# Kernel optimization log

Measured on AMD Instinct MI355X. Metric: run time of the kernel, lower is better.

The kernel has to match this reference:

```python
import jax, jax.numpy as jnp
import numpy as np

B, A, C, M = 8, 32768, 80, 32
VAR0, VAR1 = 0.1, 0.2          # cfg['variance']
TOPK = 50                      # pre_anchor_topk
T1 = 0.5                       # bbox_threshold
SL1_W, SL1_B = 0.75, 0.11      # smooth_l1_loss_param
ALPHA, GAMMA = 0.5, 2.0
EPS = 1e-12


def point_form(b):
    # center form (cx,cy,w,h) -> corner form (x0,y0,x1,y1)
    return jnp.concatenate([b[..., :2] - b[..., 2:] / 2,
                            b[..., :2] + b[..., 2:] / 2], axis=-1)


def decode(loc, priors):
    xy = priors[..., :2] + loc[..., :2] * VAR0 * priors[..., 2:]
    wh = priors[..., 2:] * jnp.exp(loc[..., 2:] * VAR1)
    return jnp.concatenate([xy, wh], axis=-1)  # center form


def encode(matched, priors):
    # matched: corner form, priors: center form
    g_xy = ((matched[..., :2] + matched[..., 2:]) / 2 - priors[..., :2]) / (VAR0 * priors[..., 2:])
    g_wh = jnp.log((matched[..., 2:] - matched[..., :2]) / priors[..., 2:]) / VAR1
    return jnp.concatenate([g_xy, g_wh], axis=-1)


def jaccard(a, b):
    # a: [M,4] corner, b: [A,4] corner -> IoU [M,A]
    lt = jnp.maximum(a[:, None, :2], b[None, :, :2])
    rb = jnp.minimum(a[:, None, 2:], b[None, :, 2:])
    wh = jnp.clip(rb - lt, 0.0, None)
    inter = wh[..., 0] * wh[..., 1]
    area_a = (a[:, 2] - a[:, 0]) * (a[:, 3] - a[:, 1])
    area_b = (b[:, 2] - b[:, 0]) * (b[:, 3] - b[:, 1])
    return inter / (area_a[:, None] + area_b[None, :] - inter)


def clip_st(x, lo):
    # Clip custom Function: straight-through gradient
    return x + jax.lax.stop_gradient(jnp.maximum(x, lo) - x)


def bce_log(x):
    # torch BCE clamps log at -100
    return jnp.maximum(jnp.log(jnp.clip(x, 1e-38, None)), -100.0)


def _per_image(box_reg, cls_p, tgt, lab, anchors, num_classes):
    # ---- image_box_prob (no-grad branch in original) ----
    decoded = point_form(decode(box_reg, anchors))          # [A,4]
    obi = jaccard(tgt, decoded)                             # [M,A]
    t2 = jnp.maximum(obi.max(axis=1, keepdims=True), T1 + EPS)
    obp = jnp.clip((obi - T1) / (t2 - T1), 0.0, 1.0)        # [M,A]
    # sparse per-class max over objects == segment_max on labels
    seg = jax.ops.segment_max(obp, lab, num_segments=num_classes)  # [C,A]
    image_box_prob = jax.lax.stop_gradient(jnp.maximum(seg, 0.0).T)  # [A,C]

    # ---- positive bag loss ----
    mq = jaccard(tgt, point_form(anchors))                  # [M,A]
    _, matched = jax.lax.top_k(mq, TOPK)                    # [M,K]
    cls_sel = cls_p[:, lab].T                               # [M,A] prob of own class
    matched_cls = jnp.take_along_axis(cls_sel, matched, axis=1)  # [M,K]
    pri = anchors[matched]                                  # [M,K,4]
    tgt_enc = encode(tgt[:, None, :], pri)                  # [M,K,4]
    val = tgt_enc - box_reg[matched]
    av = jnp.abs(val)
    reg_loss = SL1_W * jnp.where(av < SL1_B, 0.5 / SL1_B * val * val, av - 0.5 * SL1_B).sum(-1)
    logits = matched_cls * jnp.exp(-reg_loss)               # [M,K]
    w = 1.0 / clip_st(1.0 - logits, EPS)
    w = w / w.sum(axis=1, keepdims=True)
    bag = (w * logits).sum(axis=1)                          # [M]
    pos = -bce_log(bag)                                     # BCE(bag, 1)
    return image_box_prob, pos


def setup_inputs() -> dict:
    key = jax.random.key(0)
    k1, k2, k3, k4, k5, k6, k7 = jax.random.split(key, 7)
    box_regression = jax.random.normal(k1, (B, A, 4), jnp.float32) * 0.5
    cls_logits = jax.random.normal(k2, (B, A, C), jnp.float32) - 2.0
    a_xy = jax.random.uniform(k3, (A, 2))
    a_wh = 0.02 + 0.2 * jax.random.uniform(k4, (A, 2))
    anchors = jnp.concatenate([a_xy, a_wh], axis=-1).astype(jnp.float32)
    t_min = 0.5 * jax.random.uniform(k5, (B, M, 2))
    t_wh = 0.05 + 0.4 * jax.random.uniform(k6, (B, M, 2))
    target_boxes = jnp.concatenate([t_min, t_min + t_wh], axis=-1).astype(jnp.float32)
    labels = jax.random.randint(k7, (B, M), 0, C, dtype=jnp.int32)
    return {"box_regression": box_regression, "cls_logits": cls_logits,
            "anchors": anchors, "target_boxes": target_boxes, "labels": labels}


def reference(box_regression, cls_logits, anchors, target_boxes, labels):
    num_classes = cls_logits.shape[-1]
    cls_prob = jax.nn.sigmoid(cls_logits)                   # [B,A,C]
    box_prob, pos = jax.vmap(
        lambda br, cp, tb, lb: _per_image(br, cp, tb, lb, anchors, num_classes)
    )(box_regression, cls_prob, target_boxes, labels)       # [B,A,C], [B,M]
    positive_numels = target_boxes.shape[0] * target_boxes.shape[1]
    positive_loss = pos.sum() / max(1, positive_numels)
    p = cls_prob * (1.0 - box_prob)
    # focal_loss(p, gamma) = sum(p**gamma * BCE(p, 0)) = sum(p**gamma * -log(1-p))
    negative_loss = jnp.sum(p ** GAMMA * (-bce_log(1.0 - p))) / max(1, positive_numels * TOPK)
    return (positive_loss * ALPHA, negative_loss * (1.0 - ALPHA))
```

## Files before the change

### kernel.cpp

```cpp
#include <hip/hip_runtime.h>

#define NB 8
#define NA 32768
#define NC 80
#define NM 32
#define NK 50
#define CAP 2048
#define TB 32
#define HALF_A (NA / 2)
#define NBLK 1024
#define CORRB (NA / 256)
constexpr float VAR0 = 0.1f, VAR1 = 0.2f;
constexpr float T1f  = 0.5f;
constexpr float SL1B = 0.11f;
constexpr float SL1W = 0.75f;
constexpr float FEPS = 1e-12f;

__device__ __forceinline__ float iou_corner(float tx0, float ty0, float tx1, float ty1, float ta,
                                            float bx0, float by0, float bx1, float by1, float ba) {
  float lx = fmaxf(tx0, bx0), ly = fmaxf(ty0, by0);
  float rx = fminf(tx1, bx1), ry = fminf(ty1, by1);
  float wx = fmaxf(rx - lx, 0.f), wy = fmaxf(ry - ly, 0.f);
  float inter = wx * wy;
  return inter / (ta + ba - inter);
}

__device__ __forceinline__ float focal_term(float s, float bp) {
  float pr = s * (1.f - bp);
  float om = fmaxf(1.f - pr, 1e-38f);
  return pr * pr * fminf(-__logf(om), 100.f);
}

__device__ __forceinline__ float focal4(float4 v) {
  float s0 = 1.f / (1.f + __expf(-v.x));
  float s1 = 1.f / (1.f + __expf(-v.y));
  float s2 = 1.f / (1.f + __expf(-v.z));
  float s3 = 1.f / (1.f + __expf(-v.w));
  return focal_term(s0, 0.f) + focal_term(s1, 0.f) + focal_term(s2, 0.f) + focal_term(s3, 0.f);
}

__global__ void __launch_bounds__(1024, 8) mega_kernel(const float4* __restrict__ br,
                                                       const float* __restrict__ cls,
                                                       const float4* __restrict__ anc,
                                                       const float4* __restrict__ tgt,
                                                       unsigned* __restrict__ partmax,
                                                       unsigned* __restrict__ pairmask,
                                                       unsigned long long* __restrict__ cand50,
                                                       unsigned* __restrict__ poscnt,
                                                       unsigned* __restrict__ zlist,
                                                       unsigned* __restrict__ zcnt,
                                                       float* __restrict__ f0part) {
  __shared__ int hist[512];
  __shared__ unsigned long long cand[CAP];
  __shared__ int s_cnt, s_B1, s_filled, s_zc;
  __shared__ unsigned char s_flag[1024];
  __shared__ unsigned s_max[NM];
  __shared__ float4 s_t[NM];
  __shared__ float s_ta[NM];
  __shared__ float swave[16];

  int bx = blockIdx.x;
  int tid = threadIdx.x;

  {
    const float4* cls4 = (const float4*)cls;
    constexpr int STRIDE = NBLK * 1024;
    int base = bx * 1024 + tid;
    float4 v0 = cls4[base + 0 * STRIDE];
    float4 v1 = cls4[base + 1 * STRIDE];
    float4 v2 = cls4[base + 2 * STRIDE];
    float4 v3 = cls4[base + 3 * STRIDE];
    float4 v4 = cls4[base + 4 * STRIDE];
    float accum = focal4(v0) + focal4(v1) + focal4(v2) + focal4(v3) + focal4(v4);
    for (int off = 32; off; off >>= 1) accum += __shfl_down(accum, off);
    if ((tid & 63) == 0) swave[tid >> 6] = accum;
    __syncthreads();
    if (tid == 0) {
      float s = 0.f;
#pragma unroll
      for (int i = 0; i < 16; ++i) s += swave[i];
      f0part[bx] = s;
    }
    __syncthreads();
  }

  if (bx < 2 * NB * NM) {
    int bm = bx >> 1;
    int half = bx & 1;
    int abase = half * HALF_A;
    float4 t = tgt[bm];
    float ta = (t.z - t.x) * (t.w - t.y);

    if (tid < 512) hist[tid] = 0;
    if (tid == 0) s_cnt = 0;
    __syncthreads();

    float riou[16];
    unsigned mask = 0u;
#pragma unroll
    for (int k = 0; k < 16; ++k) {
      float4 p = anc[abase + tid + (k << 10)];
      float hx = 0.5f * p.z, hy = 0.5f * p.w;
      float x0 = p.x - hx, y0 = p.y - hy, x1 = p.x + hx, y1 = p.y + hy;
      float ba = (x1 - x0) * (y1 - y0);
      float v = iou_corner(t.x, t.y, t.z, t.w, ta, x0, y0, x1, y1, ba);
      riou[k] = v;
      if (v > 0.f) {
        mask |= 1u << k;
        atomicAdd(&hist[(int)(__float_as_uint(v) >> 21)], 1);
      }
    }
    __syncthreads();

    if (tid == 0) {
      int cum = 0, b1 = 0;
      for (int bin = 511; bin >= 0; --bin) {
        cum += hist[bin];
        if (cum >= NK) { b1 = bin; break; }
      }
      s_B1 = b1;
      s_filled = cum;
    }
    __syncthreads();
    int B1 = s_B1;
    int local_pos = s_filled;
    if (tid == 0) poscnt[bm * 2 + half] = (unsigned)min(local_pos, NK);

#pragma unroll
    for (int k = 0; k < 16; ++k) {
      float v = riou[k];
      if (v > 0.f) {
        unsigned vb = __float_as_uint(v);
        if ((int)(vb >> 21) >= B1) {
          int slot = atomicAdd(&s_cnt, 1);
          if (slot < CAP)
            cand[slot] = ((unsigned long long)vb << 32) | (unsigned)(~(abase + tid + (k << 10)));
        }
      }
    }
    __syncthreads();
    int n = min(s_cnt, CAP);

    for (int c = tid; c < n; c += 1024) {
      unsigned long long key = cand[c];
      int rank = 0;
      for (int j = 0; j < n; ++j) rank += (cand[j] > key);
      if (rank < NK) cand50[(size_t)(bm * 2 + half) * NK + rank] = key;
    }
    int nw = min(n, NK);
    if (tid >= nw && tid < NK)
      cand50[(size_t)(bm * 2 + half) * NK + tid] = 0ull;

    if (local_pos < NK) {
      if (tid == 0) s_zc = 0;
      __syncthreads();
#pragma unroll
      for (int k = 0; k < 16; ++k) {
        s_flag[tid] = ((mask >> k) & 1u) == 0u;
        __syncthreads();
        if (tid == 0) {
          for (int i = 0; i < 1024 && s_zc < NK; ++i)
            if (s_flag[i]) zlist[(size_t)(bm * 2 + half) * NK + s_zc++] = abase + (k << 10) + i;
        }
        __syncthreads();
      }
      if (tid == 0) zcnt[bm * 2 + half] = (unsigned)s_zc;
    }

  } else if (bx < 2 * NB * NM + TB * NB) {
    int t2i = bx - 2 * NB * NM;
    int b = t2i >> 5;
    int chunk = t2i & 31;
    if (tid < NM) {
      float4 t = tgt[b * NM + tid];
      s_t[tid] = t;
      s_ta[tid] = (t.z - t.x) * (t.w - t.y);
      s_max[tid] = 0u;
    }
    __syncthreads();

    int a = chunk * 1024 + tid;
    float4 p = anc[a];
    float4 l = br[(size_t)b * NA + a];
    float cx = p.x + l.x * VAR0 * p.z;
    float cy = p.y + l.y * VAR0 * p.w;
    float w = p.z * __expf(l.z * VAR1);
    float h = p.w * __expf(l.w * VAR1);
    float dx0 = cx - 0.5f * w, dy0 = cy - 0.5f * h;
    float dx1 = cx + 0.5f * w, dy1 = cy + 0.5f * h;
    float da = (dx1 - dx0) * (dy1 - dy0);

    unsigned mymask = 0u;
#pragma unroll
    for (int mm = 0; mm < NM; ++mm) {
      int m = (tid + mm) & (NM - 1);
      float4 t = s_t[m];
      float iou = iou_corner(t.x, t.y, t.z, t.w, s_ta[m], dx0, dy0, dx1, dy1, da);
      if (iou > T1f) mymask |= 1u << m;
      atomicMax(&s_max[m], __float_as_uint(iou));
    }
    pairmask[(size_t)b * NA + a] = mymask;
    __syncthreads();
    if (tid < NM)
      partmax[((size_t)b * NM + tid) * TB + chunk] = s_max[tid];
  }
}

__global__ void __launch_bounds__(128) posfin_kernel(const float4* __restrict__ br,
                                                     const float* __restrict__ cls,
                                                     const float4* __restrict__ anc,
                                                     const float4* __restrict__ tgt,
                                                     const int* __restrict__ labels,
                                                     const unsigned long long* __restrict__ cand50,
                                                     const unsigned* __restrict__ poscnt,
                                                     const unsigned* __restrict__ zlist,
                                                     const unsigned* __restrict__ zcnt,
                                                     float* __restrict__ posp) {
  __shared__ unsigned long long kbuf[2 * NK];
  __shared__ int sel[NK];
  __shared__ int s_total;
  int bm = blockIdx.x;
  int b = bm >> 5;
  int tid = threadIdx.x;
  float4 t = tgt[bm];

  if (tid < NK) {
    kbuf[tid]      = cand50[(size_t)(bm * 2 + 0) * NK + tid];
    kbuf[NK + tid] = cand50[(size_t)(bm * 2 + 1) * NK + tid];
  }
  if (tid == 0)
    s_total = (int)(poscnt[bm * 2] + poscnt[bm * 2 + 1]);
  __syncthreads();

  if (tid < 2 * NK) {
    unsigned long long key = kbuf[tid];
    if (key != 0ull) {
      int rank = 0;
      for (int j = 0; j < 2 * NK; ++j) rank += (kbuf[j] > key);
      if (rank < NK) sel[rank] = (int)(~(unsigned)(key & 0xFFFFFFFFull));
    }
  }
  __syncthreads();

  int total = s_total;
  if (total < NK) {
    if (tid == 0) {
      int idx = total;
      unsigned zc0 = zcnt[bm * 2], zc1 = zcnt[bm * 2 + 1];
      for (unsigned j = 0; j < zc0 && idx < NK; ++j) sel[idx++] = (int)zlist[(size_t)(bm * 2) * NK + j];
      for (unsigned j = 0; j < zc1 && idx < NK; ++j) sel[idx++] = (int)zlist[(size_t)(bm * 2 + 1) * NK + j];
    }
    __syncthreads();
  }

  if (tid < 64) {
    int lane = tid;
    float lg = 0.f, wr = 0.f;
    if (lane < NK) {
      int a = sel[lane];
      int lb = labels[bm];
      float4 p = anc[a];
      float4 l = br[(size_t)b * NA + a];
      float logit = cls[((size_t)b * NA + a) * NC + lb];
      float mc = 1.f / (1.f + __expf(-logit));
      float gx = ((t.x + t.z) * 0.5f - p.x) / (VAR0 * p.z);
      float gy = ((t.y + t.w) * 0.5f - p.y) / (VAR0 * p.w);
      float gw = __logf((t.z - t.x) / p.z) / VAR1;
      float gh = __logf((t.w - t.y) / p.w) / VAR1;
      float v0 = gx - l.x, v1 = gy - l.y, v2 = gw - l.z, v3 = gh - l.w;
      float rl = 0.f;
      {
        float av;
        av = fabsf(v0); rl += (av < SL1B) ? (0.5f / SL1B) * v0 * v0 : (av - 0.5f * SL1B);
        av = fabsf(v1); rl += (av < SL1B) ? (0.5f / SL1B) * v1 * v1 : (av - 0.5f * SL1B);
        av = fabsf(v2); rl += (av < SL1B) ? (0.5f / SL1B) * v2 * v2 : (av - 0.5f * SL1B);
        av = fabsf(v3); rl += (av < SL1B) ? (0.5f / SL1B) * v3 * v3 : (av - 0.5f * SL1B);
      }
      rl *= SL1W;
      lg = mc * __expf(-rl);
      wr = 1.f / fmaxf(1.f - lg, FEPS);
    }
    float swl = wr * lg, swr = wr;
    for (int off = 32; off; off >>= 1) { swl += __shfl_down(swl, off); swr += __shfl_down(swr, off); }
    if (lane == 0) {
      float bag = swl / swr;
      posp[bm] = -fmaxf(logf(fmaxf(bag, 1e-38f)), -100.f);
    }
  }
}

__global__ void __launch_bounds__(256) corr_kernel(const float4* __restrict__ br,
                                                   const float* __restrict__ cls,
                                                   const float4* __restrict__ anc,
                                                   const float4* __restrict__ tgt,
                                                   const int* __restrict__ labels,
                                                   const unsigned* __restrict__ partmax,
                                                   const unsigned* __restrict__ pairmask,
                                                   float* __restrict__ corrp) {
  __shared__ float4 s_t[NM];
  __shared__ float s_ta[NM], s_inv[NM];
  __shared__ unsigned s_cmask[NC];
  __shared__ unsigned s_maxm[NM];
  __shared__ unsigned s_slotmask[NM];
  __shared__ int s_slotclass[NM];
  __shared__ int s_nslots;
  int b = blockIdx.y;
  int tid = threadIdx.x;
  if (tid < NC) s_cmask[tid] = 0u;
  if (tid < NM) s_maxm[tid] = 0u;
  if (tid == 0) s_nslots = 0;
  __syncthreads();
  if (tid < NM) {
    float4 t = tgt[b * NM + tid];
    s_t[tid] = t;
    s_ta[tid] = (t.z - t.x) * (t.w - t.y);
    atomicOr(&s_cmask[labels[b * NM + tid]], 1u << tid);
  }
  {
    int m = tid >> 3, j = tid & 7;
    const unsigned* pm = &partmax[((size_t)b * NM + m) * TB];
    unsigned mx = 0u;
    for (int k = j; k < TB; k += 8) mx = max(mx, pm[k]);
    atomicMax(&s_maxm[m], mx);
  }
  __syncthreads();
  if (tid < NM) {
    float mxf = __uint_as_float(s_maxm[tid]);
    s_inv[tid] = 1.0f / (fmaxf(mxf, T1f) - T1f);
  }
  __syncthreads();
  if (tid < NC && s_cmask[tid] != 0u) {
    int slot = atomicAdd(&s_nslots, 1);
    s_slotmask[slot] = s_cmask[tid];
    s_slotclass[slot] = tid;
  }
  __syncthreads();
  int nslots = s_nslots;

  int a = blockIdx.x * 256 + tid;
  unsigned mk32 = pairmask[(size_t)b * NA + a];
  float accum = 0.f;
  if (mk32) {
    float4 p = anc[a];
    float4 l = br[(size_t)b * NA + a];
    float cx = p.x + l.x * VAR0 * p.z;
    float cy = p.y + l.y * VAR0 * p.w;
    float w = p.z * __expf(l.z * VAR1);
    float h = p.w * __expf(l.w * VAR1);
    float dx0 = cx - 0.5f * w, dy0 = cy - 0.5f * h;
    float dx1 = cx + 0.5f * w, dy1 = cy + 0.5f * h;
    float da = (dx1 - dx0) * (dy1 - dy0);
    for (int j = 0; j < nslots; ++j) {
      unsigned sm = mk32 & s_slotmask[j];
      if (!sm) continue;
      float bp = 0.f;
      while (sm) {
        int m = __ffs(sm) - 1;
        sm &= sm - 1;
        float4 t = s_t[m];
        float iou = iou_corner(t.x, t.y, t.z, t.w, s_ta[m], dx0, dy0, dx1, dy1, da);
        float o = (iou - T1f) * s_inv[m];
        bp = fmaxf(bp, fminf(fmaxf(o, 0.f), 1.f));
      }
      if (bp > 0.f) {
        float logit = cls[((size_t)b * NA + a) * NC + s_slotclass[j]];
        float s = 1.f / (1.f + __expf(-logit));
        accum += focal_term(s, bp) - focal_term(s, 0.f);
      }
    }
  }
  for (int off = 32; off; off >>= 1) accum += __shfl_down(accum, off);
  __shared__ float swv[4];
  if ((tid & 63) == 0) swv[tid >> 6] = accum;
  __syncthreads();
  if (tid == 0)
    corrp[(size_t)b * CORRB + blockIdx.x] = swv[0] + swv[1] + swv[2] + swv[3];
}

__global__ void __launch_bounds__(256) fin_kernel(const float* __restrict__ posp,
                                                  const float* __restrict__ f0part,
                                                  const float* __restrict__ corrp,
                                                  float* __restrict__ out) {
  int tid = threadIdx.x;
  double sp = 0.0, sn = 0.0;
  for (int i = tid; i < NB * NM; i += 256) sp += (double)posp[i];
  for (int i = tid; i < NBLK; i += 256) sn += (double)f0part[i];
  for (int i = tid; i < NB * CORRB; i += 256) sn += (double)corrp[i];
  for (int off = 32; off; off >>= 1) { sp += __shfl_down(sp, off); sn += __shfl_down(sn, off); }
  __shared__ double swp[4], swn[4];
  if ((tid & 63) == 0) { swp[tid >> 6] = sp; swn[tid >> 6] = sn; }
  __syncthreads();
  if (tid == 0) {
    double pos = swp[0] + swp[1] + swp[2] + swp[3];
    double neg = swn[0] + swn[1] + swn[2] + swn[3];
    out[0] = (float)(pos / 256.0 * 0.5);
    out[1] = (float)(neg / 12800.0 * 0.5);
  }
}

extern "C" void kernel_launch(void* const* d_in, const int* in_sizes, int n_in,
                              void* d_out, int out_size, void* d_ws, size_t ws_size,
                              hipStream_t stream) {
  const float4* br  = (const float4*)d_in[0];
  const float*  cls = (const float*)d_in[1];
  const float4* anc = (const float4*)d_in[2];
  const float4* tgt = (const float4*)d_in[3];
  const int*    lab = (const int*)d_in[4];
  float* out = (float*)d_out;
  float*              posp     = (float*)d_ws;
  float*              f0part   = (float*)((char*)d_ws + 4096);
  float*              corrp    = (float*)((char*)d_ws + 8192);
  unsigned*           poscnt   = (unsigned*)((char*)d_ws + 12288);
  unsigned*           partmax  = (unsigned*)((char*)d_ws + 16384);
  unsigned long long* cand50   = (unsigned long long*)((char*)d_ws + 49152);
  unsigned*           zlist    = (unsigned*)((char*)d_ws + 253952);
  unsigned*           zcnt     = (unsigned*)((char*)d_ws + 356352);
  unsigned*           pairmask = (unsigned*)((char*)d_ws + 360448);

  mega_kernel<<<dim3(NBLK), 1024, 0, stream>>>(
      br, cls, anc, tgt, partmax, pairmask, cand50, poscnt, zlist, zcnt, f0part);
  posfin_kernel<<<dim3(NB * NM), 128, 0, stream>>>(
      br, cls, anc, tgt, lab, cand50, poscnt, zlist, zcnt, posp);
  corr_kernel<<<dim3(CORRB, NB), 256, 0, stream>>>(br, cls, anc, tgt, lab, partmax, pairmask, corrp);
  fin_kernel<<<1, 256, 0, stream>>>(posp, f0part, corrp, out);
}
```

Measured before the change: 57.52 us.

## Merge four kernels into two with uniform mega blocks and last-block finalize

The mega kernel now runs 512 uniform blocks, and every block performs all three jobs: the dense focal sum over ten float4 loads per thread, decoded-box IoU for half the threads, and one top-k anchor selection. This replaces the earlier heterogeneous block roles. The positive-loss, correction and final-reduction kernels are folded into one tail kernel that accumulates into double atomics and finishes with a ticket-based last-block reduction. Candidate insertion now uses a wave ballot with one shared atomic per wave. The intent is fewer launches and better load balance, at the cost of more work serialized per block and reliance on global atomics and threadfence ordering.

```diff
diff --git a/kernel.cpp b/kernel.cpp
--- a/kernel.cpp
+++ b/kernel.cpp
@@ -6,10 +6,11 @@
 #define NM 32
 #define NK 50
 #define CAP 2048
-#define TB 32
 #define HALF_A (NA / 2)
-#define NBLK 1024
-#define CORRB (NA / 256)
+#define MBLK 512
+#define TPC 64
+#define CORR_BLOCKS (NB * 128)
+#define TAIL_BLOCKS (CORR_BLOCKS + NB * NM)
 constexpr float VAR0 = 0.1f, VAR1 = 0.2f;
 constexpr float T1f  = 0.5f;
 constexpr float SL1B = 0.11f;
@@ -49,7 +50,9 @@
                                                        unsigned* __restrict__ poscnt,
                                                        unsigned* __restrict__ zlist,
                                                        unsigned* __restrict__ zcnt,
-                                                       float* __restrict__ f0part) {
+                                                       float* __restrict__ f0part,
+                                                       double* __restrict__ acc,
+                                                       unsigned* __restrict__ ticket) {
   __shared__ int hist[512];
   __shared__ unsigned long long cand[CAP];
   __shared__ int s_cnt, s_B1, s_filled, s_zc;
@@ -62,9 +65,16 @@
   int bx = blockIdx.x;
   int tid = threadIdx.x;
 
+  if (bx == 0) {
+    if (tid < 16) acc[tid] = 0.0;
+    if (tid == 16) *ticket = 0u;
+  }
+
+  int b_img = bx >> 6;
+
   {
     const float4* cls4 = (const float4*)cls;
-    constexpr int STRIDE = NBLK * 1024;
+    constexpr int STRIDE = MBLK * 1024;
     int base = bx * 1024 + tid;
     float4 v0 = cls4[base + 0 * STRIDE];
     float4 v1 = cls4[base + 1 * STRIDE];
@@ -72,116 +82,34 @@
     float4 v3 = cls4[base + 3 * STRIDE];
     float4 v4 = cls4[base + 4 * STRIDE];
     float accum = focal4(v0) + focal4(v1) + focal4(v2) + focal4(v3) + focal4(v4);
+    float4 w0 = cls4[base + 5 * STRIDE];
+    float4 w1 = cls4[base + 6 * STRIDE];
+    float4 w2 = cls4[base + 7 * STRIDE];
+    float4 w3 = cls4[base + 8 * STRIDE];
+    float4 w4 = cls4[base + 9 * STRIDE];
+    accum += focal4(w0) + focal4(w1) + focal4(w2) + focal4(w3) + focal4(w4);
     for (int off = 32; off; off >>= 1) accum += __shfl_down(accum, off);
     if ((tid & 63) == 0) swave[tid >> 6] = accum;
-    __syncthreads();
-    if (tid == 0) {
-      float s = 0.f;
+  }
+  if (tid < NM) {
+    float4 t = tgt[b_img * NM + tid];
+    s_t[tid] = t;
+    s_ta[tid] = (t.z - t.x) * (t.w - t.y);
+    s_max[tid] = 0u;
+  }
+  __syncthreads();
+  if (tid == 0) {
+    float s = 0.f;
 #pragma unroll
-      for (int i = 0; i < 16; ++i) s += swave[i];
-      f0part[bx] = s;
-    }
-    __syncthreads();
-  }
-
-  if (bx < 2 * NB * NM) {
-    int bm = bx >> 1;
-    int half = bx & 1;
-    int abase = half * HALF_A;
-    float4 t = tgt[bm];
-    float ta = (t.z - t.x) * (t.w - t.y);
-
-    if (tid < 512) hist[tid] = 0;
-    if (tid == 0) s_cnt = 0;
-    __syncthreads();
-
-    float riou[16];
-    unsigned mask = 0u;
-#pragma unroll
-    for (int k = 0; k < 16; ++k) {
-      float4 p = anc[abase + tid + (k << 10)];
-      float hx = 0.5f * p.z, hy = 0.5f * p.w;
-      float x0 = p.x - hx, y0 = p.y - hy, x1 = p.x + hx, y1 = p.y + hy;
-      float ba = (x1 - x0) * (y1 - y0);
-      float v = iou_corner(t.x, t.y, t.z, t.w, ta, x0, y0, x1, y1, ba);
-      riou[k] = v;
-      if (v > 0.f) {
-        mask |= 1u << k;
-        atomicAdd(&hist[(int)(__float_as_uint(v) >> 21)], 1);
-      }
-    }
-    __syncthreads();
-
-    if (tid == 0) {
-      int cum = 0, b1 = 0;
-      for (int bin = 511; bin >= 0; --bin) {
-        cum += hist[bin];
-        if (cum >= NK) { b1 = bin; break; }
-      }
-      s_B1 = b1;
-      s_filled = cum;
-    }
-    __syncthreads();
-    int B1 = s_B1;
-    int local_pos = s_filled;
-    if (tid == 0) poscnt[bm * 2 + half] = (unsigned)min(local_pos, NK);
-
-#pragma unroll
-    for (int k = 0; k < 16; ++k) {
-      float v = riou[k];
-      if (v > 0.f) {
-        unsigned vb = __float_as_uint(v);
-        if ((int)(vb >> 21) >= B1) {
-          int slot = atomicAdd(&s_cnt, 1);
-          if (slot < CAP)
-            cand[slot] = ((unsigned long long)vb << 32) | (unsigned)(~(abase + tid + (k << 10)));
-        }
-      }
-    }
-    __syncthreads();
-    int n = min(s_cnt, CAP);
-
-    for (int c = tid; c < n; c += 1024) {
-      unsigned long long key = cand[c];
-      int rank = 0;
-      for (int j = 0; j < n; ++j) rank += (cand[j] > key);
-      if (rank < NK) cand50[(size_t)(bm * 2 + half) * NK + rank] = key;
-    }
-    int nw = min(n, NK);
-    if (tid >= nw && tid < NK)
-      cand50[(size_t)(bm * 2 + half) * NK + tid] = 0ull;
-
-    if (local_pos < NK) {
-      if (tid == 0) s_zc = 0;
-      __syncthreads();
-#pragma unroll
-      for (int k = 0; k < 16; ++k) {
-        s_flag[tid] = ((mask >> k) & 1u) == 0u;
-        __syncthreads();
-        if (tid == 0) {
-          for (int i = 0; i < 1024 && s_zc < NK; ++i)
-            if (s_flag[i]) zlist[(size_t)(bm * 2 + half) * NK + s_zc++] = abase + (k << 10) + i;
-        }
-        __syncthreads();
-      }
-      if (tid == 0) zcnt[bm * 2 + half] = (unsigned)s_zc;
-    }
-
-  } else if (bx < 2 * NB * NM + TB * NB) {
-    int t2i = bx - 2 * NB * NM;
-    int b = t2i >> 5;
-    int chunk = t2i & 31;
-    if (tid < NM) {
-      float4 t = tgt[b * NM + tid];
-      s_t[tid] = t;
-      s_ta[tid] = (t.z - t.x) * (t.w - t.y);
-      s_max[tid] = 0u;
-    }
-    __syncthreads();
-
-    int a = chunk * 1024 + tid;
+    for (int i = 0; i < 16; ++i) s += swave[i];
+    f0part[bx] = s;
+  }
+
+  if (tid >= 512) {
+    int g = bx * 512 + (tid - 512);
+    int a = g & (NA - 1);
     float4 p = anc[a];
-    float4 l = br[(size_t)b * NA + a];
+    float4 l = br[g];
     float cx = p.x + l.x * VAR0 * p.z;
     float cy = p.y + l.y * VAR0 * p.w;
     float w = p.z * __expf(l.z * VAR1);
@@ -189,7 +117,6 @@
     float dx0 = cx - 0.5f * w, dy0 = cy - 0.5f * h;
     float dx1 = cx + 0.5f * w, dy1 = cy + 0.5f * h;
     float da = (dx1 - dx0) * (dy1 - dy0);
-
     unsigned mymask = 0u;
 #pragma unroll
     for (int mm = 0; mm < NM; ++mm) {
@@ -199,202 +126,297 @@
       if (iou > T1f) mymask |= 1u << m;
       atomicMax(&s_max[m], __float_as_uint(iou));
     }
-    pairmask[(size_t)b * NA + a] = mymask;
-    __syncthreads();
-    if (tid < NM)
-      partmax[((size_t)b * NM + tid) * TB + chunk] = s_max[tid];
-  }
-}
-
-__global__ void __launch_bounds__(128) posfin_kernel(const float4* __restrict__ br,
-                                                     const float* __restrict__ cls,
-                                                     const float4* __restrict__ anc,
-                                                     const float4* __restrict__ tgt,
-                                                     const int* __restrict__ labels,
-                                                     const unsigned long long* __restrict__ cand50,
-                                                     const unsigned* __restrict__ poscnt,
-                                                     const unsigned* __restrict__ zlist,
-                                                     const unsigned* __restrict__ zcnt,
-                                                     float* __restrict__ posp) {
-  __shared__ unsigned long long kbuf[2 * NK];
-  __shared__ int sel[NK];
-  __shared__ int s_total;
-  int bm = blockIdx.x;
-  int b = bm >> 5;
-  int tid = threadIdx.x;
+    pairmask[g] = mymask;
+  }
+  if (tid < 512) hist[tid] = 0;
+  if (tid == 0) s_cnt = 0;
+  __syncthreads();
+  if (tid < NM)
+    partmax[((size_t)b_img * NM + tid) * TPC + (bx & 63)] = s_max[tid];
+
+  int bm = bx >> 1;
+  int half = bx & 1;
+  int abase = half * HALF_A;
   float4 t = tgt[bm];
-
-  if (tid < NK) {
-    kbuf[tid]      = cand50[(size_t)(bm * 2 + 0) * NK + tid];
-    kbuf[NK + tid] = cand50[(size_t)(bm * 2 + 1) * NK + tid];
-  }
-  if (tid == 0)
-    s_total = (int)(poscnt[bm * 2] + poscnt[bm * 2 + 1]);
-  __syncthreads();
-
-  if (tid < 2 * NK) {
-    unsigned long long key = kbuf[tid];
-    if (key != 0ull) {
-      int rank = 0;
-      for (int j = 0; j < 2 * NK; ++j) rank += (kbuf[j] > key);
-      if (rank < NK) sel[rank] = (int)(~(unsigned)(key & 0xFFFFFFFFull));
-    }
-  }
-  __syncthreads();
-
-  int total = s_total;
-  if (total < NK) {
-    if (tid == 0) {
-      int idx = total;
-      unsigned zc0 = zcnt[bm * 2], zc1 = zcnt[bm * 2 + 1];
-      for (unsigned j = 0; j < zc0 && idx < NK; ++j) sel[idx++] = (int)zlist[(size_t)(bm * 2) * NK + j];
-      for (unsigned j = 0; j < zc1 && idx < NK; ++j) sel[idx++] = (int)zlist[(size_t)(bm * 2 + 1) * NK + j];
-    }
-    __syncthreads();
-  }
-
-  if (tid < 64) {
-    int lane = tid;
-    float lg = 0.f, wr = 0.f;
-    if (lane < NK) {
-      int a = sel[lane];
-      int lb = labels[bm];
-      float4 p = anc[a];
-      float4 l = br[(size_t)b * NA + a];
-      float logit = cls[((size_t)b * NA + a) * NC + lb];
-      float mc = 1.f / (1.f + __expf(-logit));
-      float gx = ((t.x + t.z) * 0.5f - p.x) / (VAR0 * p.z);
-      float gy = ((t.y + t.w) * 0.5f - p.y) / (VAR0 * p.w);
-      float gw = __logf((t.z - t.x) / p.z) / VAR1;
-      float gh = __logf((t.w - t.y) / p.w) / VAR1;
-      float v0 = gx - l.x, v1 = gy - l.y, v2 = gw - l.z, v3 = gh - l.w;
-      float rl = 0.f;
-      {
-        float av;
-        av = fabsf(v0); rl += (av < SL1B) ? (0.5f / SL1B) * v0 * v0 : (av - 0.5f * SL1B);
-        av = fabsf(v1); rl += (av < SL1B) ? (0.5f / SL1B) * v1 * v1 : (av - 0.5f * SL1B);
-        av = fabsf(v2); rl += (av < SL1B) ? (0.5f / SL1B) * v2 * v2 : (av - 0.5f * SL1B);
-        av = fabsf(v3); rl += (av < SL1B) ? (0.5f / SL1B) * v3 * v3 : (av - 0.5f * SL1B);
-      }
-      rl *= SL1W;
-      lg = mc * __expf(-rl);
-      wr = 1.f / fmaxf(1.f - lg, FEPS);
-    }
-    float swl = wr * lg, swr = wr;
-    for (int off = 32; off; off >>= 1) { swl += __shfl_down(swl, off); swr += __shfl_down(swr, off); }
-    if (lane == 0) {
-      float bag = swl / swr;
-      posp[bm] = -fmaxf(logf(fmaxf(bag, 1e-38f)), -100.f);
-    }
-  }
-}
-
-__global__ void __launch_bounds__(256) corr_kernel(const float4* __restrict__ br,
+  float ta = (t.z - t.x) * (t.w - t.y);
+
+  float riou[16];
+  unsigned mask = 0u;
+#pragma unroll
+  for (int k = 0; k < 16; ++k) {
+    float4 p = anc[abase + tid + (k << 10)];
+    float hx = 0.5f * p.z, hy = 0.5f * p.w;
+    float x0 = p.x - hx, y0 = p.y - hy, x1 = p.x + hx, y1 = p.y + hy;
+    float ba = (x1 - x0) * (y1 - y0);
+    float v = iou_corner(t.x, t.y, t.z, t.w, ta, x0, y0, x1, y1, ba);
+    riou[k] = v;
+    if (v > 0.f) {
+      mask |= 1u << k;
+      atomicAdd(&hist[(int)(__float_as_uint(v) >> 21)], 1);
+    }
+  }
+  __syncthreads();
+
+  if (tid == 0) {
+    int cum = 0, b1 = 0;
+    for (int bin = 511; bin >= 0; --bin) {
+      cum += hist[bin];
+      if (cum >= NK) { b1 = bin; break; }
+    }
+    s_B1 = b1;
+    s_filled = cum;
+  }
+  __syncthreads();
+  int B1 = s_B1;
+  int local_pos = s_filled;
+  if (tid == 0) poscnt[bm * 2 + half] = (unsigned)min(local_pos, NK);
+
+  int lane = tid & 63;
+#pragma unroll
+  for (int k = 0; k < 16; ++k) {
+    float v = riou[k];
+    bool want = (v > 0.f) && ((int)(__float_as_uint(v) >> 21) >= B1);
+    unsigned long long ball = __ballot(want);
+    if (ball) {
+      int lead = __ffsll((long long)ball) - 1;
+      int base = 0;
+      if (lane == lead) base = atomicAdd(&s_cnt, __popcll(ball));
+      base = __shfl(base, lead);
+      if (want) {
+        int slot = base + __popcll(ball & ((1ull << lane) - 1ull));
+        if (slot < CAP)
+          cand[slot] = ((unsigned long long)__float_as_uint(v) << 32)
+                       | (unsigned)(~(abase + tid + (k << 10)));
+      }
+    }
+  }
+  __syncthreads();
+  int n = min(s_cnt, CAP);
+
+  for (int c = tid; c < n; c += 1024) {
+    unsigned long long key = cand[c];
+    int rank = 0;
+    for (int j = 0; j < n; ++j) rank += (cand[j] > key);
+    if (rank < NK) cand50[(size_t)(bm * 2 + half) * NK + rank] = key;
+  }
+  int nw = min(n, NK);
+  if (tid >= nw && tid < NK)
+    cand50[(size_t)(bm * 2 + half) * NK + tid] = 0ull;
+
+  if (local_pos < NK) {
+    if (tid == 0) s_zc = 0;
+    __syncthreads();
+#pragma unroll
+    for (int k = 0; k < 16; ++k) {
+      s_flag[tid] = ((mask >> k) & 1u) == 0u;
+      __syncthreads();
+      if (tid == 0) {
+        for (int i = 0; i < 1024 && s_zc < NK; ++i)
+          if (s_flag[i]) zlist[(size_t)(bm * 2 + half) * NK + s_zc++] = abase + (k << 10) + i;
+      }
+      __syncthreads();
+    }
+    if (tid == 0) zcnt[bm * 2 + half] = (unsigned)s_zc;
+  }
+}
+
+__global__ void __launch_bounds__(256) tail_kernel(const float4* __restrict__ br,
                                                    const float* __restrict__ cls,
                                                    const float4* __restrict__ anc,
                                                    const float4* __restrict__ tgt,
                                                    const int* __restrict__ labels,
                                                    const unsigned* __restrict__ partmax,
                                                    const unsigned* __restrict__ pairmask,
-                                                   float* __restrict__ corrp) {
-  __shared__ float4 s_t[NM];
-  __shared__ float s_ta[NM], s_inv[NM];
-  __shared__ unsigned s_cmask[NC];
-  __shared__ unsigned s_maxm[NM];
-  __shared__ unsigned s_slotmask[NM];
-  __shared__ int s_slotclass[NM];
-  __shared__ int s_nslots;
-  int b = blockIdx.y;
+                                                   const unsigned long long* __restrict__ cand50,
+                                                   const unsigned* __restrict__ poscnt,
+                                                   const unsigned* __restrict__ zlist,
+                                                   const unsigned* __restrict__ zcnt,
+                                                   const float* __restrict__ f0part,
+                                                   double* __restrict__ acc,
+                                                   unsigned* __restrict__ ticket,
+                                                   float* __restrict__ out) {
+  __shared__ int s_last;
+  int bx = blockIdx.x;
   int tid = threadIdx.x;
-  if (tid < NC) s_cmask[tid] = 0u;
-  if (tid < NM) s_maxm[tid] = 0u;
-  if (tid == 0) s_nslots = 0;
-  __syncthreads();
-  if (tid < NM) {
-    float4 t = tgt[b * NM + tid];
-    s_t[tid] = t;
-    s_ta[tid] = (t.z - t.x) * (t.w - t.y);
-    atomicOr(&s_cmask[labels[b * NM + tid]], 1u << tid);
-  }
-  {
-    int m = tid >> 3, j = tid & 7;
-    const unsigned* pm = &partmax[((size_t)b * NM + m) * TB];
-    unsigned mx = 0u;
-    for (int k = j; k < TB; k += 8) mx = max(mx, pm[k]);
-    atomicMax(&s_maxm[m], mx);
-  }
-  __syncthreads();
-  if (tid < NM) {
-    float mxf = __uint_as_float(s_maxm[tid]);
-    s_inv[tid] = 1.0f / (fmaxf(mxf, T1f) - T1f);
-  }
-  __syncthreads();
-  if (tid < NC && s_cmask[tid] != 0u) {
-    int slot = atomicAdd(&s_nslots, 1);
-    s_slotmask[slot] = s_cmask[tid];
-    s_slotclass[slot] = tid;
-  }
-  __syncthreads();
-  int nslots = s_nslots;
-
-  int a = blockIdx.x * 256 + tid;
-  unsigned mk32 = pairmask[(size_t)b * NA + a];
-  float accum = 0.f;
-  if (mk32) {
-    float4 p = anc[a];
-    float4 l = br[(size_t)b * NA + a];
-    float cx = p.x + l.x * VAR0 * p.z;
-    float cy = p.y + l.y * VAR0 * p.w;
-    float w = p.z * __expf(l.z * VAR1);
-    float h = p.w * __expf(l.w * VAR1);
-    float dx0 = cx - 0.5f * w, dy0 = cy - 0.5f * h;
-    float dx1 = cx + 0.5f * w, dy1 = cy + 0.5f * h;
-    float da = (dx1 - dx0) * (dy1 - dy0);
-    for (int j = 0; j < nslots; ++j) {
-      unsigned sm = mk32 & s_slotmask[j];
-      if (!sm) continue;
-      float bp = 0.f;
-      while (sm) {
-        int m = __ffs(sm) - 1;
-        sm &= sm - 1;
-        float4 t = s_t[m];
-        float iou = iou_corner(t.x, t.y, t.z, t.w, s_ta[m], dx0, dy0, dx1, dy1, da);
-        float o = (iou - T1f) * s_inv[m];
-        bp = fmaxf(bp, fminf(fmaxf(o, 0.f), 1.f));
-      }
-      if (bp > 0.f) {
-        float logit = cls[((size_t)b * NA + a) * NC + s_slotclass[j]];
-        float s = 1.f / (1.f + __expf(-logit));
-        accum += focal_term(s, bp) - focal_term(s, 0.f);
-      }
-    }
-  }
-  for (int off = 32; off; off >>= 1) accum += __shfl_down(accum, off);
-  __shared__ float swv[4];
-  if ((tid & 63) == 0) swv[tid >> 6] = accum;
-  __syncthreads();
-  if (tid == 0)
-    corrp[(size_t)b * CORRB + blockIdx.x] = swv[0] + swv[1] + swv[2] + swv[3];
-}
-
-__global__ void __launch_bounds__(256) fin_kernel(const float* __restrict__ posp,
-                                                  const float* __restrict__ f0part,
-                                                  const float* __restrict__ corrp,
-                                                  float* __restrict__ out) {
-  int tid = threadIdx.x;
-  double sp = 0.0, sn = 0.0;
-  for (int i = tid; i < NB * NM; i += 256) sp += (double)posp[i];
-  for (int i = tid; i < NBLK; i += 256) sn += (double)f0part[i];
-  for (int i = tid; i < NB * CORRB; i += 256) sn += (double)corrp[i];
-  for (int off = 32; off; off >>= 1) { sp += __shfl_down(sp, off); sn += __shfl_down(sn, off); }
-  __shared__ double swp[4], swn[4];
-  if ((tid & 63) == 0) { swp[tid >> 6] = sp; swn[tid >> 6] = sn; }
-  __syncthreads();
+
+  if (bx < CORR_BLOCKS) {
+    __shared__ float4 s_t[NM];
+    __shared__ float s_ta[NM], s_inv[NM];
+    __shared__ unsigned s_cmask[NC];
+    __shared__ unsigned s_maxm[NM];
+    __shared__ unsigned s_slotmask[NM];
+    __shared__ int s_slotclass[NM];
+    __shared__ int s_nslots;
+    int b = bx >> 7;
+    if (tid < NC) s_cmask[tid] = 0u;
+    if (tid < NM) s_maxm[tid] = 0u;
+    if (tid == 0) s_nslots = 0;
+    __syncthreads();
+    if (tid < NM) {
+      float4 t = tgt[b * NM + tid];
+      s_t[tid] = t;
+      s_ta[tid] = (t.z - t.x) * (t.w - t.y);
+      atomicOr(&s_cmask[labels[b * NM + tid]], 1u << tid);
+    }
+    {
+      int m = tid >> 3, j = tid & 7;
+      const unsigned* pm = &partmax[((size_t)b * NM + m) * TPC];
+      unsigned mx = 0u;
+      for (int k = j; k < TPC; k += 8) mx = max(mx, pm[k]);
+      atomicMax(&s_maxm[m], mx);
+    }
+    __syncthreads();
+    if (tid < NM) {
+      float mxf = __uint_as_float(s_maxm[tid]);
+      s_inv[tid] = 1.0f / (fmaxf(mxf, T1f) - T1f);
+    }
+    __syncthreads();
+    if (tid < NC && s_cmask[tid] != 0u) {
+      int slot = atomicAdd(&s_nslots, 1);
+      s_slotmask[slot] = s_cmask[tid];
+      s_slotclass[slot] = tid;
+    }
+    __syncthreads();
+    int nslots = s_nslots;
+
+    int a = (bx & 127) * 256 + tid;
+    unsigned mk32 = pairmask[(size_t)b * NA + a];
+    float accum = 0.f;
+    if (mk32) {
+      float4 p = anc[a];
+      float4 l = br[(size_t)b * NA + a];
+      float cx = p.x + l.x * VAR0 * p.z;
+      float cy = p.y + l.y * VAR0 * p.w;
+      float w = p.z * __expf(l.z * VAR1);
+      float h = p.w * __expf(l.w * VAR1);
+      float dx0 = cx - 0.5f * w, dy0 = cy - 0.5f * h;
+      float dx1 = cx + 0.5f * w, dy1 = cy + 0.5f * h;
+      float da = (dx1 - dx0) * (dy1 - dy0);
+      for (int j = 0; j < nslots; ++j) {
+        unsigned sm = mk32 & s_slotmask[j];
+        if (!sm) continue;
+        float bp = 0.f;
+        while (sm) {
+          int m = __ffs(sm) - 1;
+          sm &= sm - 1;
+          float4 t = s_t[m];
+          float iou = iou_corner(t.x, t.y, t.z, t.w, s_ta[m], dx0, dy0, dx1, dy1, da);
+          float o = (iou - T1f) * s_inv[m];
+          bp = fmaxf(bp, fminf(fmaxf(o, 0.f), 1.f));
+        }
+        if (bp > 0.f) {
+          float logit = cls[((size_t)b * NA + a) * NC + s_slotclass[j]];
+          float s = 1.f / (1.f + __expf(-logit));
+          accum += focal_term(s, bp) - focal_term(s, 0.f);
+        }
+      }
+    }
+    for (int off = 32; off; off >>= 1) accum += __shfl_down(accum, off);
+    __shared__ float swv[4];
+    if ((tid & 63) == 0) swv[tid >> 6] = accum;
+    __syncthreads();
+    if (tid == 0) {
+      float tot = swv[0] + swv[1] + swv[2] + swv[3];
+      if (tot != 0.f) atomicAdd(&acc[bx & 7], (double)tot);
+    }
+
+  } else {
+    __shared__ unsigned long long kbuf[2 * NK];
+    __shared__ int sel[NK];
+    __shared__ int s_total;
+    int bm = bx - CORR_BLOCKS;
+    int b = bm >> 5;
+    float4 t = tgt[bm];
+
+    if (tid < NK) {
+      kbuf[tid]      = cand50[(size_t)(bm * 2 + 0) * NK + tid];
+      kbuf[NK + tid] = cand50[(size_t)(bm * 2 + 1) * NK + tid];
+    }
+    if (tid == 0)
+      s_total = (int)(poscnt[bm * 2] + poscnt[bm * 2 + 1]);
+    __syncthreads();
+
+    if (tid < 2 * NK) {
+      unsigned long long key = kbuf[tid];
+      if (key != 0ull) {
+        int rank = 0;
+        for (int j = 0; j < 2 * NK; ++j) rank += (kbuf[j] > key);
+        if (rank < NK) sel[rank] = (int)(~(unsigned)(key & 0xFFFFFFFFull));
+      }
+    }
+    __syncthreads();
+
+    int total = s_total;
+    if (total < NK) {
+      if (tid == 0) {
+        int idx = total;
+        unsigned zc0 = zcnt[bm * 2], zc1 = zcnt[bm * 2 + 1];
+        for (unsigned j = 0; j < zc0 && idx < NK; ++j) sel[idx++] = (int)zlist[(size_t)(bm * 2) * NK + j];
+        for (unsigned j = 0; j < zc1 && idx < NK; ++j) sel[idx++] = (int)zlist[(size_t)(bm * 2 + 1) * NK + j];
+      }
+      __syncthreads();
+    }
+
+    if (tid < 64) {
+      int lane = tid;
+      float lg = 0.f, wr = 0.f;
+      if (lane < NK) {
+        int a = sel[lane];
+        int lb = labels[bm];
+        float4 p = anc[a];
+        float4 l = br[(size_t)b * NA + a];
+        float logit = cls[((size_t)b * NA + a) * NC + lb];
+        float mc = 1.f / (1.f + __expf(-logit));
+        float gx = ((t.x + t.z) * 0.5f - p.x) / (VAR0 * p.z);
+        float gy = ((t.y + t.w) * 0.5f - p.y) / (VAR0 * p.w);
+        float gw = __logf((t.z - t.x) / p.z) / VAR1;
+        float gh = __logf((t.w - t.y) / p.w) / VAR1;
+        float v0 = gx - l.x, v1 = gy - l.y, v2 = gw - l.z, v3 = gh - l.w;
+        float rl = 0.f;
+        {
+          float av;
+          av = fabsf(v0); rl += (av < SL1B) ? (0.5f / SL1B) * v0 * v0 : (av - 0.5f * SL1B);
+          av = fabsf(v1); rl += (av < SL1B) ? (0.5f / SL1B) * v1 * v1 : (av - 0.5f * SL1B);
+          av = fabsf(v2); rl += (av < SL1B) ? (0.5f / SL1B) * v2 * v2 : (av - 0.5f * SL1B);
+          av = fabsf(v3); rl += (av < SL1B) ? (0.5f / SL1B) * v3 * v3 : (av - 0.5f * SL1B);
+        }
+        rl *= SL1W;
+        lg = mc * __expf(-rl);
+        wr = 1.f / fmaxf(1.f - lg, FEPS);
+      }
+      float swl = wr * lg, swr = wr;
+      for (int off = 32; off; off >>= 1) { swl += __shfl_down(swl, off); swr += __shfl_down(swr, off); }
+      if (lane == 0) {
+        float bag = swl / swr;
+        float pos = -fmaxf(logf(fmaxf(bag, 1e-38f)), -100.f);
+        atomicAdd(&acc[8 + (bm & 7)], (double)pos);
+      }
+    }
+  }
+
   if (tid == 0) {
-    double pos = swp[0] + swp[1] + swp[2] + swp[3];
-    double neg = swn[0] + swn[1] + swn[2] + swn[3];
-    out[0] = (float)(pos / 256.0 * 0.5);
-    out[1] = (float)(neg / 12800.0 * 0.5);
+    __threadfence();
+    unsigned tk = atomicAdd(ticket, 1u);
+    s_last = (tk == TAIL_BLOCKS - 1) ? 1 : 0;
+  }
+  __syncthreads();
+  if (s_last) {
+    double sn = 0.0;
+    for (int i = tid; i < MBLK; i += 256) sn += (double)f0part[i];
+    for (int off = 32; off; off >>= 1) sn += __shfl_down(sn, off);
+    __shared__ double swn[4];
+    if ((tid & 63) == 0) swn[tid >> 6] = sn;
+    __syncthreads();
+    if (tid == 0) {
+      double neg = swn[0] + swn[1] + swn[2] + swn[3];
+      double pos = 0.0;
+      for (int i = 0; i < 8; ++i) {
+        neg += atomicAdd(&acc[i], 0.0);
+        pos += atomicAdd(&acc[8 + i], 0.0);
+      }
+      out[0] = (float)(pos / 256.0 * 0.5);
+      out[1] = (float)(neg / 12800.0 * 0.5);
+    }
   }
 }
 
@@ -407,20 +429,19 @@
   const float4* tgt = (const float4*)d_in[3];
   const int*    lab = (const int*)d_in[4];
   float* out = (float*)d_out;
-  float*              posp     = (float*)d_ws;
-  float*              f0part   = (float*)((char*)d_ws + 4096);
-  float*              corrp    = (float*)((char*)d_ws + 8192);
-  unsigned*           poscnt   = (unsigned*)((char*)d_ws + 12288);
+  float*              f0part   = (float*)d_ws;
+  unsigned*           poscnt   = (unsigned*)((char*)d_ws + 4096);
+  double*             acc      = (double*)((char*)d_ws + 8192);
+  unsigned*           ticket   = (unsigned*)((char*)d_ws + 8320);
   unsigned*           partmax  = (unsigned*)((char*)d_ws + 16384);
-  unsigned long long* cand50   = (unsigned long long*)((char*)d_ws + 49152);
-  unsigned*           zlist    = (unsigned*)((char*)d_ws + 253952);
-  unsigned*           zcnt     = (unsigned*)((char*)d_ws + 356352);
-  unsigned*           pairmask = (unsigned*)((char*)d_ws + 360448);
-
-  mega_kernel<<<dim3(NBLK), 1024, 0, stream>>>(
-      br, cls, anc, tgt, partmax, pairmask, cand50, poscnt, zlist, zcnt, f0part);
-  posfin_kernel<<<dim3(NB * NM), 128, 0, stream>>>(
-      br, cls, anc, tgt, lab, cand50, poscnt, zlist, zcnt, posp);
-  corr_kernel<<<dim3(CORRB, NB), 256, 0, stream>>>(br, cls, anc, tgt, lab, partmax, pairmask, corrp);
-  fin_kernel<<<1, 256, 0, stream>>>(posp, f0part, corrp, out);
-}
+  unsigned long long* cand50   = (unsigned long long*)((char*)d_ws + 81920);
+  unsigned*           zlist    = (unsigned*)((char*)d_ws + 286720);
+  unsigned*           zcnt     = (unsigned*)((char*)d_ws + 389120);
+  unsigned*           pairmask = (unsigned*)((char*)d_ws + 393216);
+
+  mega_kernel<<<dim3(MBLK), 1024, 0, stream>>>(
+      br, cls, anc, tgt, partmax, pairmask, cand50, poscnt, zlist, zcnt, f0part, acc, ticket);
+  tail_kernel<<<dim3(TAIL_BLOCKS), 256, 0, stream>>>(
+      br, cls, anc, tgt, lab, partmax, pairmask, cand50, poscnt, zlist, zcnt,
+      f0part, acc, ticket, out);
+}
```

After: 79.56 us. +38.3%, slower.
